# Optimization experiments

Hardware: AMD Instinct MI355X
Metric: run time of the kernel (lower is better)

The kernel has to match this reference:

```python
import jax, jax.numpy as jnp
import numpy as np
import math

WIDTH = 1024
DATA_WIDTH = 1024
HEADS = 16


def setup_inputs() -> dict:
    key = jax.random.key(0)
    ks = jax.random.split(key, 8)
    bs, n_ctx, n_data = 2, 1024, 4096
    init_scale = 0.25 / math.sqrt(WIDTH)
    inp = {
        "x": jax.random.normal(ks[0], (bs, n_ctx, WIDTH), dtype=jnp.float32),
        "data": jax.random.normal(ks[1], (bs, n_data, DATA_WIDTH), dtype=jnp.float32),
        "Wq": jax.random.normal(ks[2], (WIDTH, WIDTH), dtype=jnp.float32) * init_scale,
        "bq": jnp.zeros((WIDTH,), dtype=jnp.float32),
        "Wkv": jax.random.normal(ks[3], (DATA_WIDTH, 2 * WIDTH), dtype=jnp.float32) * init_scale,
        "bkv": jnp.zeros((2 * WIDTH,), dtype=jnp.float32),
        "Wproj": jax.random.normal(ks[4], (WIDTH, WIDTH), dtype=jnp.float32) * init_scale,
        "bproj": jnp.zeros((WIDTH,), dtype=jnp.float32),
    }
    return inp


def reference(x, data, Wq, bq, Wkv, bkv, Wproj, bproj):
    bs, n_ctx, _ = x.shape
    _, n_data, _ = data.shape
    h = HEADS
    attn_ch = WIDTH // h  # = (2*width)//heads//2
    scale = 1.0 / math.sqrt(math.sqrt(attn_ch))

    q = x @ Wq + bq                      # [bs, n_ctx, width]
    kv = data @ Wkv + bkv                # [bs, n_data, 2*width]

    q = q.reshape(bs, n_ctx, h, attn_ch)
    kv = kv.reshape(bs, n_data, h, 2 * attn_ch)
    k, v = kv[..., :attn_ch], kv[..., attn_ch:]

    # full O(n_ctx * n_data) attention weights, softmax in fp32 (faithful to use_flash=False path)
    weight = jnp.einsum('bthc,bshc->bhts', q * scale, k * scale)
    wdtype = weight.dtype
    weight = jax.nn.softmax(weight.astype(jnp.float32), axis=-1).astype(wdtype)
    out = jnp.einsum('bhts,bshc->bthc', weight, v).reshape(bs, n_ctx, WIDTH)

    return out @ Wproj + bproj
```

## Files before the change

### kernel.cpp

```cpp
#include <hip/hip_runtime.h>
#include <hip/hip_bf16.h>


typedef __bf16 bf16;
typedef float f32x4 __attribute__((ext_vector_type(4)));
typedef bf16 bf16x4 __attribute__((ext_vector_type(4)));
typedef bf16 bf16x8 __attribute__((ext_vector_type(8)));

#define MFMA16(A, B, C) __builtin_amdgcn_mfma_f32_16x16x32_bf16((A), (B), (C), 0, 0, 0)

constexpr int BS = 2;
constexpr int NCTX = 1024;
constexpr int NDATA = 4096;
constexpr int WID = 1024;
constexpr int NH = 16;
constexpr int DH = 64;
constexpr int NSPLIT = 4;
constexpr float ATT_SCALE = 0.35355339059327373f;

__device__ __forceinline__ void gload16(const void* g, void* l) {
  __builtin_amdgcn_global_load_lds(
      (const __attribute__((address_space(1))) unsigned int*)g,
      (__attribute__((address_space(3))) unsigned int*)l, 16, 0, 0);
}

__global__ __launch_bounds__(256) void convert_kernel(
    const float* __restrict__ x, const float* __restrict__ data,
    bf16* __restrict__ x16, bf16* __restrict__ d16) {
  const int bid = blockIdx.x;
  const float* src;
  bf16* dst;
  size_t i;
  if (bid < 1024) {
    src = x; dst = x16; i = ((size_t)bid * 256 + threadIdx.x) * 8;
  } else {
    src = data; dst = d16; i = ((size_t)(bid - 1024) * 256 + threadIdx.x) * 8;
  }
  float4 v0 = *reinterpret_cast<const float4*>(&src[i]);
  float4 v1 = *reinterpret_cast<const float4*>(&src[i + 4]);
  bf16x8 o;
  o[0] = (bf16)v0.x; o[1] = (bf16)v0.y; o[2] = (bf16)v0.z; o[3] = (bf16)v0.w;
  o[4] = (bf16)v1.x; o[5] = (bf16)v1.y; o[6] = (bf16)v1.z; o[7] = (bf16)v1.w;
  *reinterpret_cast<bf16x8*>(&dst[i]) = o;
}

__global__ __launch_bounds__(256) void transpose_all_kernel(
    const float* __restrict__ Wq, const float* __restrict__ Wkv,
    const float* __restrict__ Wproj, bf16* __restrict__ wqT,
    bf16* __restrict__ wkvT, bf16* __restrict__ wprojT) {
  __shared__ float tile[64][65];
  const int bid = blockIdx.x, tid = threadIdx.x;
  const float* in;
  bf16* out;
  int R = 1024, C, cx, ry;
  if (bid < 256) {
    in = Wq; out = wqT; C = 1024; cx = bid & 15; ry = bid >> 4;
  } else if (bid < 768) {
    int t = bid - 256; in = Wkv; out = wkvT; C = 2048; cx = t & 31; ry = t >> 5;
  } else {
    int t = bid - 768; in = Wproj; out = wprojT; C = 1024; cx = t & 15; ry = t >> 4;
  }
  const int c0 = cx * 64, r0 = ry * 64;
#pragma unroll
  for (int i = 0; i < 16; ++i) {
    int idx = tid + i * 256;
    int row = idx >> 6, col = idx & 63;
    tile[row][col] = in[(size_t)(r0 + row) * C + (c0 + col)];
  }
  __syncthreads();
#pragma unroll
  for (int i = 0; i < 16; ++i) {
    int idx = tid + i * 256;
    int orow = idx >> 6, ocol = idx & 63;
    out[(size_t)(c0 + orow) * R + (r0 + ocol)] = (bf16)tile[ocol][orow];
  }
}

#define GEMM_MAINLOOP(Aptr, Bptr)                                              \
  __shared__ bf16 As[128][32];                                                 \
  __shared__ bf16 Bs[128][32];                                                 \
  const int tid = threadIdx.x, lane = tid & 63, w = tid >> 6;                  \
  const int wm = (w & 1) * 64, wn = (w >> 1) * 64;                             \
  const int l15 = lane & 15, l4 = lane >> 4;                                   \
  const int srow = w * 32 + (lane >> 2);                                       \
  const int scolb = (lane & 3) * 16;                                           \
  const char* a_src = (const char*)((Aptr) + (size_t)(m0 + srow) * 1024) + scolb; \
  const char* b_src = (const char*)((Bptr) + (size_t)(n0 + srow) * 1024) + scolb; \
  bf16* lds_a0 = &As[w * 32][0];                                               \
  bf16* lds_a1 = &As[w * 32 + 16][0];                                          \
  bf16* lds_b0 = &Bs[w * 32][0];                                               \
  bf16* lds_b1 = &Bs[w * 32 + 16][0];                                          \
  f32x4 acc[4][4] = {};                                                        \
  for (int kt = 0; kt < 32; ++kt) {                                            \
    __syncthreads();                                                           \
    gload16(a_src + kt * 64, lds_a0);                                          \
    gload16(a_src + kt * 64 + 16 * 2048, lds_a1);                              \
    gload16(b_src + kt * 64, lds_b0);                                          \
    gload16(b_src + kt * 64 + 16 * 2048, lds_b1);                              \
    __syncthreads();                                                           \
    bf16x8 af[4], bfr[4];                                                      \
    _Pragma("unroll") for (int mi = 0; mi < 4; ++mi)                           \
        af[mi] = *reinterpret_cast<const bf16x8*>(&As[wm + mi * 16 + l15][l4 * 8]); \
    _Pragma("unroll") for (int ni = 0; ni < 4; ++ni)                           \
        bfr[ni] = *reinterpret_cast<const bf16x8*>(&Bs[wn + ni * 16 + l15][l4 * 8]); \
    _Pragma("unroll") for (int mi = 0; mi < 4; ++mi)                           \
        _Pragma("unroll") for (int ni = 0; ni < 4; ++ni)                       \
            acc[mi][ni] = MFMA16(af[mi], bfr[ni], acc[mi][ni]);                \
  }

__global__ __launch_bounds__(256) void gemm_q_kernel(
    const bf16* __restrict__ X, const bf16* __restrict__ WT,
    const float* __restrict__ bias, bf16* __restrict__ Q) {
  const int nt = blockIdx.x & 7, mt = blockIdx.x >> 3;
  const int m0 = mt * 128, n0 = nt * 128;
  GEMM_MAINLOOP(X, WT)
#pragma unroll
  for (int ni = 0; ni < 4; ++ni) {
    int n = n0 + wn + ni * 16 + l15;
    float bv = bias[n];
    int h = n >> 6, d = n & 63;
#pragma unroll
    for (int mi = 0; mi < 4; ++mi)
#pragma unroll
      for (int r = 0; r < 4; ++r) {
        int m = m0 + wm + mi * 16 + l4 * 4 + r;
        int b = m >> 10, t = m & 1023;
        Q[(((size_t)(b * NH + h)) * NCTX + t) * DH + d] =
            (bf16)((acc[mi][ni][r] + bv) * ATT_SCALE);
      }
  }
}

__global__ __launch_bounds__(256) void gemm_kv_kernel(
    const bf16* __restrict__ DATA, const bf16* __restrict__ WT,
    const float* __restrict__ bias, bf16* __restrict__ Kb,
    bf16* __restrict__ Vt) {
  const int nt = blockIdx.x & 15, mt = blockIdx.x >> 4;
  const int m0 = mt * 128, n0 = nt * 128;
  GEMM_MAINLOOP(DATA, WT)
#pragma unroll
  for (int ni = 0; ni < 4; ++ni) {
    int n = n0 + wn + ni * 16 + l15;
    float bv = bias[n];
    int h = n >> 7, c = n & 127;
#pragma unroll
    for (int mi = 0; mi < 4; ++mi)
#pragma unroll
      for (int r = 0; r < 4; ++r) {
        int m = m0 + wm + mi * 16 + l4 * 4 + r;
        int b = m >> 12, s = m & 4095;
        float vv = acc[mi][ni][r] + bv;
        if (c < DH) {
          Kb[(((size_t)(b * NH + h)) * NDATA + s) * DH + c] = (bf16)(vv * ATT_SCALE);
        } else {
          Vt[(((size_t)(b * NH + h)) * DH + (c - DH)) * NDATA + s] = (bf16)vv;
        }
      }
  }
}

__global__ __launch_bounds__(256) void gemm_proj_kernel(
    const bf16* __restrict__ A, const bf16* __restrict__ WT,
    const float* __restrict__ bias, float* __restrict__ OUT) {
  const int nt = blockIdx.x & 7, mt = blockIdx.x >> 3;
  const int m0 = mt * 128, n0 = nt * 128;
  GEMM_MAINLOOP(A, WT)
#pragma unroll
  for (int ni = 0; ni < 4; ++ni) {
    int n = n0 + wn + ni * 16 + l15;
    float bv = bias[n];
#pragma unroll
    for (int mi = 0; mi < 4; ++mi)
#pragma unroll
      for (int r = 0; r < 4; ++r) {
        int m = m0 + wm + mi * 16 + l4 * 4 + r;
        OUT[(size_t)m * 1024 + n] = acc[mi][ni][r] + bv;
      }
  }
}

__global__ __launch_bounds__(256) void attn_kernel(
    const bf16* __restrict__ Q,
    const bf16* __restrict__ Kb,
    const bf16* __restrict__ Vt,
    bf16* __restrict__ Op,
    float* __restrict__ Ls) {
  constexpr int SCH = 32;
  constexpr int NIT = (NDATA / NSPLIT) / SCH;
  __shared__ bf16 Ks[2][32][64];
  __shared__ bf16 Vs[2][64][32];
  const int tid = threadIdx.x, lane = tid & 63, w = tid >> 6;
  const int wg = (blockIdx.x & 7) * 256 + (blockIdx.x >> 3);
  const int tt = wg & 15, sp = (wg >> 4) & 3, h = (wg >> 6) & 15, b = wg >> 10;
  const int t0 = tt * 64 + w * 16;
  const int l15 = lane & 15, l4 = lane >> 4;
  const size_t qbase = (((size_t)(b * NH + h)) * NCTX + t0) * DH;
  const size_t kbase = ((size_t)(b * NH + h)) * NDATA * DH;
  const size_t vbase = ((size_t)(b * NH + h)) * DH * NDATA;

  bf16x8 qf0 = *reinterpret_cast<const bf16x8*>(&Q[qbase + (size_t)l15 * DH + l4 * 8]);
  bf16x8 qf1 = *reinterpret_cast<const bf16x8*>(&Q[qbase + (size_t)l15 * DH + 32 + l4 * 8]);

  const int krow0 = ((l15 >> 2) << 3) + (l15 & 3);
  const int kf_swz = ((l15 & 3) | (((l15 >> 2) & 1) << 2)) << 4;
  const int koff_a = ((l4 * 16) ^ kf_swz) >> 1;
  const int koff_b = ((64 + l4 * 16) ^ kf_swz) >> 1;
  const int voff = ((l4 * 16) ^ ((l15 & 3) << 4)) >> 1;

  const int kst_off = (w * 8 + (lane >> 3)) * 128 +
      (((lane & 7) * 16) ^ (((((lane >> 3) & 3)) | ((w & 1) << 2)) << 4));
  const int vrow_g = w * 16 + (lane >> 2);
  const char* vrowp = (const char*)(Vt + vbase + (size_t)vrow_g * NDATA);
  const int vst_coff = ((lane & 3) * 16) ^ ((((lane >> 2) & 3)) << 4);
  const char* kchunk = (const char*)(Kb + kbase);

  f32x4 o[4] = {};
  float lsum = 0.f;

  const int sstart = sp * (NDATA / NSPLIT);
  gload16(kchunk + (size_t)sstart * 128 + kst_off, &Ks[0][w * 8][0]);
  gload16(vrowp + (size_t)sstart * 2 + vst_coff, &Vs[0][w * 16][0]);
  __syncthreads();

  int cur = 0;
  for (int it = 0; it < NIT; ++it) {
    const int s0 = sstart + it * SCH;
    if (it + 1 < NIT) {
      gload16(kchunk + (size_t)(s0 + SCH) * 128 + kst_off, &Ks[cur ^ 1][w * 8][0]);
      gload16(vrowp + (size_t)(s0 + SCH) * 2 + vst_coff, &Vs[cur ^ 1][w * 16][0]);
    }
    f32x4 p0 = {}, p1 = {};
    {
      bf16x8 a00 = *reinterpret_cast<const bf16x8*>(&Ks[cur][krow0][koff_a]);
      bf16x8 a01 = *reinterpret_cast<const bf16x8*>(&Ks[cur][krow0][koff_b]);
      p0 = MFMA16(a00, qf0, p0);
      p0 = MFMA16(a01, qf1, p0);
      bf16x8 a10 = *reinterpret_cast<const bf16x8*>(&Ks[cur][krow0 + 4][koff_a]);
      bf16x8 a11 = *reinterpret_cast<const bf16x8*>(&Ks[cur][krow0 + 4][koff_b]);
      p1 = MFMA16(a10, qf0, p1);
      p1 = MFMA16(a11, qf1, p1);
    }
    bf16x8 paf;
#pragma unroll
    for (int r = 0; r < 4; ++r) {
      float e = __expf(p0[r]);
      lsum += e;
      paf[r] = (bf16)e;
    }
#pragma unroll
    for (int r = 0; r < 4; ++r) {
      float e = __expf(p1[r]);
      lsum += e;
      paf[4 + r] = (bf16)e;
    }
#pragma unroll
    for (int dg = 0; dg < 4; ++dg) {
      bf16x8 vf = *reinterpret_cast<const bf16x8*>(&Vs[cur][dg * 16 + l15][voff]);
      o[dg] = MFMA16(paf, vf, o[dg]);
    }
    __syncthreads();
    cur ^= 1;
  }

  const size_t obase = (((size_t)((sp * BS + b) * NH + h)) * NCTX + t0);
  lsum += __shfl_xor(lsum, 16, 64);
  lsum += __shfl_xor(lsum, 32, 64);
  if (l4 == 0) Ls[obase + l15] = lsum;
#pragma unroll
  for (int dg = 0; dg < 4; ++dg)
#pragma unroll
    for (int r = 0; r < 4; ++r)
      Op[(obase + l4 * 4 + r) * DH + dg * 16 + l15] = (bf16)o[dg][r];
}

__global__ __launch_bounds__(256) void attn_combine_kernel(
    const bf16* __restrict__ Op, const float* __restrict__ Ls,
    bf16* __restrict__ AO) {
  const int idx = blockIdx.x * 256 + threadIdx.x;
  const int d = idx & 63;
  const int t = (idx >> 6) & (NCTX - 1);
  const int h = (idx >> 16) & (NH - 1);
  const int b = idx >> 20;
  float os = 0.f, ls = 0.f;
#pragma unroll
  for (int p = 0; p < NSPLIT; ++p) {
    size_t base = ((size_t)((p * BS + b) * NH + h)) * NCTX + t;
    os += (float)Op[base * DH + d];
    ls += Ls[base];
  }
  AO[((size_t)b * NCTX + t) * WID + h * DH + d] = (bf16)(os / ls);
}

extern "C" void kernel_launch(void* const* d_in, const int* in_sizes, int n_in,
                              void* d_out, int out_size, void* d_ws, size_t ws_size,
                              hipStream_t stream) {
  const float* x = (const float*)d_in[0];
  const float* data = (const float*)d_in[1];
  const float* Wq = (const float*)d_in[2];
  const float* bq = (const float*)d_in[3];
  const float* Wkv = (const float*)d_in[4];
  const float* bkv = (const float*)d_in[5];
  const float* Wproj = (const float*)d_in[6];
  const float* bproj = (const float*)d_in[7];
  float* out = (float*)d_out;

  char* ws = (char*)d_ws;
  size_t off = 0;
  auto alloc = [&](size_t bytes) -> void* {
    void* p = ws + off;
    off += (bytes + 255) & ~(size_t)255;
    return p;
  };
  bf16* d16 = (bf16*)alloc((size_t)BS * NDATA * WID * 2);
  bf16* x16 = (bf16*)alloc((size_t)BS * NCTX * WID * 2);
  bf16* qbuf = (bf16*)alloc((size_t)BS * NH * NCTX * DH * 2);
  bf16* kbuf = (bf16*)alloc((size_t)BS * NH * NDATA * DH * 2);
  bf16* vt = (bf16*)alloc((size_t)BS * NH * DH * NDATA * 2);
  bf16* wqT = (bf16*)alloc((size_t)WID * WID * 2);
  bf16* wkvT = (bf16*)alloc((size_t)2 * WID * WID * 2);
  bf16* wprojT = (bf16*)alloc((size_t)WID * WID * 2);
  float* lsbuf = (float*)alloc((size_t)NSPLIT * BS * NH * NCTX * 4);
  bf16* opbuf = d16;
  bf16* aobuf = x16;

  convert_kernel<<<dim3(1024 + 4096), 256, 0, stream>>>(x, data, x16, d16);
  transpose_all_kernel<<<dim3(1024), 256, 0, stream>>>(Wq, Wkv, Wproj, wqT, wkvT, wprojT);

  gemm_q_kernel<<<dim3((BS * NCTX / 128) * (WID / 128)), 256, 0, stream>>>(x16, wqT, bq, qbuf);
  gemm_kv_kernel<<<dim3((BS * NDATA / 128) * (2 * WID / 128)), 256, 0, stream>>>(
      d16, wkvT, bkv, kbuf, vt);
  attn_kernel<<<dim3(BS * NH * (NCTX / 64) * NSPLIT), 256, 0, stream>>>(
      qbuf, kbuf, vt, opbuf, lsbuf);
  attn_combine_kernel<<<dim3(BS * NCTX * WID / 256), 256, 0, stream>>>(opbuf, lsbuf, aobuf);
  gemm_proj_kernel<<<dim3((BS * NCTX / 128) * (WID / 128)), 256, 0, stream>>>(
      aobuf, wprojT, bproj, out);
}
```

Baseline: 266.2 us.

## Rework projection GEMMs: merge prep kernels, smaller Q/proj tiles, pipelined KV GEMM

Merges the fp32-to-bf16 conversion and weight transpose into a single prep launch. The Q and output-projection GEMMs switch to 64x128 tiles so they launch 256 workgroups instead of 128, which fills more compute units. The KV GEMM becomes a 512-thread, 256x256-tile kernel with double-buffered, XOR-swizzled LDS staging, explicit vmcnt waits and MFMA priority hints, so global loads overlap compute and tiles get more reuse. In exchange the KV kernel uses heavy LDS and registers, and correctness depends on hand-written waitcnt and swizzle logic.

```diff
diff --git a/kernel.cpp b/kernel.cpp
--- a/kernel.cpp
+++ b/kernel.cpp
@@ -4,7 +4,6 @@
 
 typedef __bf16 bf16;
 typedef float f32x4 __attribute__((ext_vector_type(4)));
-typedef bf16 bf16x4 __attribute__((ext_vector_type(4)));
 typedef bf16 bf16x8 __attribute__((ext_vector_type(8)));
 
 #define MFMA16(A, B, C) __builtin_amdgcn_mfma_f32_16x16x32_bf16((A), (B), (C), 0, 0, 0)
@@ -24,41 +23,41 @@
       (__attribute__((address_space(3))) unsigned int*)l, 16, 0, 0);
 }
 
-__global__ __launch_bounds__(256) void convert_kernel(
+__global__ __launch_bounds__(256) void prep_kernel(
     const float* __restrict__ x, const float* __restrict__ data,
-    bf16* __restrict__ x16, bf16* __restrict__ d16) {
-  const int bid = blockIdx.x;
-  const float* src;
-  bf16* dst;
-  size_t i;
-  if (bid < 1024) {
-    src = x; dst = x16; i = ((size_t)bid * 256 + threadIdx.x) * 8;
-  } else {
-    src = data; dst = d16; i = ((size_t)(bid - 1024) * 256 + threadIdx.x) * 8;
-  }
-  float4 v0 = *reinterpret_cast<const float4*>(&src[i]);
-  float4 v1 = *reinterpret_cast<const float4*>(&src[i + 4]);
-  bf16x8 o;
-  o[0] = (bf16)v0.x; o[1] = (bf16)v0.y; o[2] = (bf16)v0.z; o[3] = (bf16)v0.w;
-  o[4] = (bf16)v1.x; o[5] = (bf16)v1.y; o[6] = (bf16)v1.z; o[7] = (bf16)v1.w;
-  *reinterpret_cast<bf16x8*>(&dst[i]) = o;
-}
-
-__global__ __launch_bounds__(256) void transpose_all_kernel(
     const float* __restrict__ Wq, const float* __restrict__ Wkv,
-    const float* __restrict__ Wproj, bf16* __restrict__ wqT,
-    bf16* __restrict__ wkvT, bf16* __restrict__ wprojT) {
+    const float* __restrict__ Wproj, bf16* __restrict__ x16,
+    bf16* __restrict__ d16, bf16* __restrict__ wqT, bf16* __restrict__ wkvT,
+    bf16* __restrict__ wprojT) {
   __shared__ float tile[64][65];
   const int bid = blockIdx.x, tid = threadIdx.x;
+  if (bid < 5120) {
+    const float* src;
+    bf16* dst;
+    size_t i;
+    if (bid < 1024) {
+      src = x; dst = x16; i = ((size_t)bid * 256 + tid) * 8;
+    } else {
+      src = data; dst = d16; i = ((size_t)(bid - 1024) * 256 + tid) * 8;
+    }
+    float4 v0 = *reinterpret_cast<const float4*>(&src[i]);
+    float4 v1 = *reinterpret_cast<const float4*>(&src[i + 4]);
+    bf16x8 o;
+    o[0] = (bf16)v0.x; o[1] = (bf16)v0.y; o[2] = (bf16)v0.z; o[3] = (bf16)v0.w;
+    o[4] = (bf16)v1.x; o[5] = (bf16)v1.y; o[6] = (bf16)v1.z; o[7] = (bf16)v1.w;
+    *reinterpret_cast<bf16x8*>(&dst[i]) = o;
+    return;
+  }
+  const int t = bid - 5120;
   const float* in;
   bf16* out;
   int R = 1024, C, cx, ry;
-  if (bid < 256) {
-    in = Wq; out = wqT; C = 1024; cx = bid & 15; ry = bid >> 4;
-  } else if (bid < 768) {
-    int t = bid - 256; in = Wkv; out = wkvT; C = 2048; cx = t & 31; ry = t >> 5;
+  if (t < 256) {
+    in = Wq; out = wqT; C = 1024; cx = t & 15; ry = t >> 4;
+  } else if (t < 768) {
+    int u = t - 256; in = Wkv; out = wkvT; C = 2048; cx = u & 31; ry = u >> 5;
   } else {
-    int t = bid - 768; in = Wproj; out = wprojT; C = 1024; cx = t & 15; ry = t >> 4;
+    int u = t - 768; in = Wproj; out = wprojT; C = 1024; cx = u & 15; ry = u >> 4;
   }
   const int c0 = cx * 64, r0 = ry * 64;
 #pragma unroll
@@ -76,34 +75,29 @@
   }
 }
 
-#define GEMM_MAINLOOP(Aptr, Bptr)                                              \
-  __shared__ bf16 As[128][32];                                                 \
+#define GEMM64x128_LOOP(Aptr, Bptr)                                            \
+  __shared__ bf16 As[64][32];                                                  \
   __shared__ bf16 Bs[128][32];                                                 \
   const int tid = threadIdx.x, lane = tid & 63, w = tid >> 6;                  \
-  const int wm = (w & 1) * 64, wn = (w >> 1) * 64;                             \
+  const int wm = (w & 1) * 32, wn = (w >> 1) * 64;                             \
   const int l15 = lane & 15, l4 = lane >> 4;                                   \
-  const int srow = w * 32 + (lane >> 2);                                       \
-  const int scolb = (lane & 3) * 16;                                           \
-  const char* a_src = (const char*)((Aptr) + (size_t)(m0 + srow) * 1024) + scolb; \
-  const char* b_src = (const char*)((Bptr) + (size_t)(n0 + srow) * 1024) + scolb; \
-  bf16* lds_a0 = &As[w * 32][0];                                               \
-  bf16* lds_a1 = &As[w * 32 + 16][0];                                          \
-  bf16* lds_b0 = &Bs[w * 32][0];                                               \
-  bf16* lds_b1 = &Bs[w * 32 + 16][0];                                          \
-  f32x4 acc[4][4] = {};                                                        \
+  const int sr = lane >> 2, sc = (lane & 3) * 8;                               \
+  const bf16* a_s = (Aptr) + (((size_t)(m0 + w * 16 + sr)) << 10) + sc;        \
+  const bf16* b_s0 = (Bptr) + (((size_t)(n0 + w * 32 + sr)) << 10) + sc;       \
+  const bf16* b_s1 = (Bptr) + (((size_t)(n0 + w * 32 + 16 + sr)) << 10) + sc;  \
+  f32x4 acc[2][4] = {};                                                        \
   for (int kt = 0; kt < 32; ++kt) {                                            \
     __syncthreads();                                                           \
-    gload16(a_src + kt * 64, lds_a0);                                          \
-    gload16(a_src + kt * 64 + 16 * 2048, lds_a1);                              \
-    gload16(b_src + kt * 64, lds_b0);                                          \
-    gload16(b_src + kt * 64 + 16 * 2048, lds_b1);                              \
+    gload16(a_s + kt * 32, &As[w * 16][0]);                                    \
+    gload16(b_s0 + kt * 32, &Bs[w * 32][0]);                                   \
+    gload16(b_s1 + kt * 32, &Bs[w * 32 + 16][0]);                              \
     __syncthreads();                                                           \
-    bf16x8 af[4], bfr[4];                                                      \
-    _Pragma("unroll") for (int mi = 0; mi < 4; ++mi)                           \
+    bf16x8 af[2], bfr[4];                                                      \
+    _Pragma("unroll") for (int mi = 0; mi < 2; ++mi)                           \
         af[mi] = *reinterpret_cast<const bf16x8*>(&As[wm + mi * 16 + l15][l4 * 8]); \
     _Pragma("unroll") for (int ni = 0; ni < 4; ++ni)                           \
         bfr[ni] = *reinterpret_cast<const bf16x8*>(&Bs[wn + ni * 16 + l15][l4 * 8]); \
-    _Pragma("unroll") for (int mi = 0; mi < 4; ++mi)                           \
+    _Pragma("unroll") for (int mi = 0; mi < 2; ++mi)                           \
         _Pragma("unroll") for (int ni = 0; ni < 4; ++ni)                       \
             acc[mi][ni] = MFMA16(af[mi], bfr[ni], acc[mi][ni]);                \
   }
@@ -112,15 +106,15 @@
     const bf16* __restrict__ X, const bf16* __restrict__ WT,
     const float* __restrict__ bias, bf16* __restrict__ Q) {
   const int nt = blockIdx.x & 7, mt = blockIdx.x >> 3;
-  const int m0 = mt * 128, n0 = nt * 128;
-  GEMM_MAINLOOP(X, WT)
+  const int m0 = mt * 64, n0 = nt * 128;
+  GEMM64x128_LOOP(X, WT)
 #pragma unroll
   for (int ni = 0; ni < 4; ++ni) {
     int n = n0 + wn + ni * 16 + l15;
     float bv = bias[n];
     int h = n >> 6, d = n & 63;
 #pragma unroll
-    for (int mi = 0; mi < 4; ++mi)
+    for (int mi = 0; mi < 2; ++mi)
 #pragma unroll
       for (int r = 0; r < 4; ++r) {
         int m = m0 + wm + mi * 16 + l4 * 4 + r;
@@ -131,23 +125,132 @@
   }
 }
 
-__global__ __launch_bounds__(256) void gemm_kv_kernel(
-    const bf16* __restrict__ DATA, const bf16* __restrict__ WT,
-    const float* __restrict__ bias, bf16* __restrict__ Kb,
-    bf16* __restrict__ Vt) {
-  const int nt = blockIdx.x & 15, mt = blockIdx.x >> 4;
-  const int m0 = mt * 128, n0 = nt * 128;
-  GEMM_MAINLOOP(DATA, WT)
+__global__ __launch_bounds__(256) void gemm_proj_kernel(
+    const bf16* __restrict__ A, const bf16* __restrict__ WT,
+    const float* __restrict__ bias, float* __restrict__ OUT) {
+  const int nt = blockIdx.x & 7, mt = blockIdx.x >> 3;
+  const int m0 = mt * 64, n0 = nt * 128;
+  GEMM64x128_LOOP(A, WT)
 #pragma unroll
   for (int ni = 0; ni < 4; ++ni) {
     int n = n0 + wn + ni * 16 + l15;
     float bv = bias[n];
-    int h = n >> 7, c = n & 127;
-#pragma unroll
-    for (int mi = 0; mi < 4; ++mi)
+#pragma unroll
+    for (int mi = 0; mi < 2; ++mi)
 #pragma unroll
       for (int r = 0; r < 4; ++r) {
         int m = m0 + wm + mi * 16 + l4 * 4 + r;
+        OUT[(size_t)m * 1024 + n] = acc[mi][ni][r] + bv;
+      }
+  }
+}
+
+__global__ __launch_bounds__(512) void gemm_kv_kernel(
+    const bf16* __restrict__ DATA,
+    const bf16* __restrict__ WT,
+    const float* __restrict__ bias,
+    bf16* __restrict__ Kb,
+    bf16* __restrict__ Vt) {
+  __shared__ bf16 As[2][2][128][64];
+  __shared__ bf16 Bs[2][2][128][64];
+  const int tid = threadIdx.x, lane = tid & 63, w = tid >> 6;
+  const int l15 = lane & 15, l4 = lane >> 4;
+  const int wg = (blockIdx.x & 7) * 32 + (blockIdx.x >> 3);
+  const int nt = wg & 7, mt = wg >> 3;
+  const int m0 = mt * 256, n0 = nt * 256;
+  const int wr = w >> 2, wc = w & 3;
+
+  const int rA = tid >> 3;
+  const int cgs = ((tid & 7) ^ (rA & 7)) << 3;
+  const bf16* a_src0 = DATA + (((size_t)(m0 + rA)) << 10) + cgs;
+  const bf16* a_src1 = DATA + (((size_t)(m0 + 128 + rA)) << 10) + cgs;
+  const bf16* b_src0 = WT + (((size_t)(n0 + rA)) << 10) + cgs;
+  const bf16* b_src1 = WT + (((size_t)(n0 + 128 + rA)) << 10) + cgs;
+
+#define STAGE_A(t_, d_)                                                  \
+  gload16(a_src0 + (t_) * 64, &As[d_][0][8 * w][0]);                     \
+  gload16(a_src0 + (t_) * 64 + (64 << 10), &As[d_][0][64 + 8 * w][0]);   \
+  gload16(a_src1 + (t_) * 64, &As[d_][1][8 * w][0]);                     \
+  gload16(a_src1 + (t_) * 64 + (64 << 10), &As[d_][1][64 + 8 * w][0]);
+#define STAGE_B(t_, d_)                                                  \
+  gload16(b_src0 + (t_) * 64, &Bs[d_][0][8 * w][0]);                     \
+  gload16(b_src0 + (t_) * 64 + (64 << 10), &Bs[d_][0][64 + 8 * w][0]);   \
+  gload16(b_src1 + (t_) * 64, &Bs[d_][1][8 * w][0]);                     \
+  gload16(b_src1 + (t_) * 64 + (64 << 10), &Bs[d_][1][64 + 8 * w][0]);
+
+  const int sw = (l15 & 7) << 4;
+  const int koff0 = (((l4 << 4)) ^ sw) >> 1;
+  const int koff1 = ((64 + (l4 << 4)) ^ sw) >> 1;
+  const bf16* Arow = &As[0][wr][l15][0];
+  const bf16* Brow = &Bs[0][wc >> 1][(wc & 1) * 64 + l15][0];
+  const int dstrideA = 2 * 128 * 64;
+
+#define LDA(d_, mi, koff_) \
+  (*reinterpret_cast<const bf16x8*>(Arow + (d_) * dstrideA + (mi) * 1024 + (koff_)))
+#define LDB(d_, ni, koff_) \
+  (*reinterpret_cast<const bf16x8*>(Brow + (d_) * dstrideA + (ni) * 1024 + (koff_)))
+
+  f32x4 acc[8][4] = {};
+
+  STAGE_A(0, 0)
+  STAGE_B(0, 0)
+
+  for (int t = 0; t < 16; ++t) {
+    const int d = t & 1;
+    if (t < 15) {
+      STAGE_A(t + 1, d ^ 1)
+      asm volatile("s_waitcnt vmcnt(4)" ::: "memory");
+    } else {
+      asm volatile("s_waitcnt vmcnt(0)" ::: "memory");
+    }
+    __builtin_amdgcn_s_barrier();
+    asm volatile("" ::: "memory");
+    if (t < 15) { STAGE_B(t + 1, d ^ 1) }
+    bf16x8 bf00 = LDB(d, 0, koff0), bf01 = LDB(d, 0, koff1);
+    bf16x8 bf10 = LDB(d, 1, koff0), bf11 = LDB(d, 1, koff1);
+    bf16x8 bf20 = LDB(d, 2, koff0), bf21 = LDB(d, 2, koff1);
+    bf16x8 bf30 = LDB(d, 3, koff0), bf31 = LDB(d, 3, koff1);
+#pragma unroll
+    for (int p = 0; p < 4; ++p) {
+      bf16x8 a00 = LDA(d, 2 * p, koff0), a01 = LDA(d, 2 * p, koff1);
+      bf16x8 a10 = LDA(d, 2 * p + 1, koff0), a11 = LDA(d, 2 * p + 1, koff1);
+      __builtin_amdgcn_s_setprio(1);
+      acc[2 * p][0] = MFMA16(a00, bf00, acc[2 * p][0]);
+      acc[2 * p][0] = MFMA16(a01, bf01, acc[2 * p][0]);
+      acc[2 * p][1] = MFMA16(a00, bf10, acc[2 * p][1]);
+      acc[2 * p][1] = MFMA16(a01, bf11, acc[2 * p][1]);
+      acc[2 * p][2] = MFMA16(a00, bf20, acc[2 * p][2]);
+      acc[2 * p][2] = MFMA16(a01, bf21, acc[2 * p][2]);
+      acc[2 * p][3] = MFMA16(a00, bf30, acc[2 * p][3]);
+      acc[2 * p][3] = MFMA16(a01, bf31, acc[2 * p][3]);
+      acc[2 * p + 1][0] = MFMA16(a10, bf00, acc[2 * p + 1][0]);
+      acc[2 * p + 1][0] = MFMA16(a11, bf01, acc[2 * p + 1][0]);
+      acc[2 * p + 1][1] = MFMA16(a10, bf10, acc[2 * p + 1][1]);
+      acc[2 * p + 1][1] = MFMA16(a11, bf11, acc[2 * p + 1][1]);
+      acc[2 * p + 1][2] = MFMA16(a10, bf20, acc[2 * p + 1][2]);
+      acc[2 * p + 1][2] = MFMA16(a11, bf21, acc[2 * p + 1][2]);
+      acc[2 * p + 1][3] = MFMA16(a10, bf30, acc[2 * p + 1][3]);
+      acc[2 * p + 1][3] = MFMA16(a11, bf31, acc[2 * p + 1][3]);
+      __builtin_amdgcn_s_setprio(0);
+    }
+    asm volatile("" ::: "memory");
+    __builtin_amdgcn_s_barrier();
+  }
+#undef STAGE_A
+#undef STAGE_B
+#undef LDA
+#undef LDB
+
+#pragma unroll
+  for (int ni = 0; ni < 4; ++ni) {
+    int n = n0 + wc * 64 + ni * 16 + l15;
+    float bv = bias[n];
+    int h = n >> 7, c = n & 127;
+#pragma unroll
+    for (int mi = 0; mi < 8; ++mi)
+#pragma unroll
+      for (int r = 0; r < 4; ++r) {
+        int m = m0 + wr * 128 + mi * 16 + l4 * 4 + r;
         int b = m >> 12, s = m & 4095;
         float vv = acc[mi][ni][r] + bv;
         if (c < DH) {
@@ -155,26 +258,6 @@
         } else {
           Vt[(((size_t)(b * NH + h)) * DH + (c - DH)) * NDATA + s] = (bf16)vv;
         }
-      }
-  }
-}
-
-__global__ __launch_bounds__(256) void gemm_proj_kernel(
-    const bf16* __restrict__ A, const bf16* __restrict__ WT,
-    const float* __restrict__ bias, float* __restrict__ OUT) {
-  const int nt = blockIdx.x & 7, mt = blockIdx.x >> 3;
-  const int m0 = mt * 128, n0 = nt * 128;
-  GEMM_MAINLOOP(A, WT)
-#pragma unroll
-  for (int ni = 0; ni < 4; ++ni) {
-    int n = n0 + wn + ni * 16 + l15;
-    float bv = bias[n];
-#pragma unroll
-    for (int mi = 0; mi < 4; ++mi)
-#pragma unroll
-      for (int r = 0; r < 4; ++r) {
-        int m = m0 + wm + mi * 16 + l4 * 4 + r;
-        OUT[(size_t)m * 1024 + n] = acc[mi][ni][r] + bv;
       }
   }
 }
@@ -323,15 +406,12 @@
   bf16* opbuf = d16;
   bf16* aobuf = x16;
 
-  convert_kernel<<<dim3(1024 + 4096), 256, 0, stream>>>(x, data, x16, d16);
-  transpose_all_kernel<<<dim3(1024), 256, 0, stream>>>(Wq, Wkv, Wproj, wqT, wkvT, wprojT);
-
-  gemm_q_kernel<<<dim3((BS * NCTX / 128) * (WID / 128)), 256, 0, stream>>>(x16, wqT, bq, qbuf);
-  gemm_kv_kernel<<<dim3((BS * NDATA / 128) * (2 * WID / 128)), 256, 0, stream>>>(
-      d16, wkvT, bkv, kbuf, vt);
+  prep_kernel<<<dim3(6144), 256, 0, stream>>>(x, data, Wq, Wkv, Wproj,
+                                              x16, d16, wqT, wkvT, wprojT);
+  gemm_q_kernel<<<dim3(256), 256, 0, stream>>>(x16, wqT, bq, qbuf);
+  gemm_kv_kernel<<<dim3(256), 512, 0, stream>>>(d16, wkvT, bkv, kbuf, vt);
   attn_kernel<<<dim3(BS * NH * (NCTX / 64) * NSPLIT), 256, 0, stream>>>(
       qbuf, kbuf, vt, opbuf, lsbuf);
   attn_combine_kernel<<<dim3(BS * NCTX * WID / 256), 256, 0, stream>>>(opbuf, lsbuf, aobuf);
-  gemm_proj_kernel<<<dim3((BS * NCTX / 128) * (WID / 128)), 256, 0, stream>>>(
-      aobuf, wprojT, bproj, out);
-}
+  gemm_proj_kernel<<<dim3(256), 256, 0, stream>>>(aobuf, wprojT, bproj, out);
+}
```

New measurement: 256.9 us. 1.04x faster.
